# Kernel optimization log

Hardware: AMD Instinct MI355X
Metric: run time of the kernel (lower is better)

The kernel has to match this reference:

```python
import jax, jax.numpy as jnp
import numpy as np
from jax import lax

S = 20      # max_segments
D = 1000    # traj_dict entries
L = 200     # dmp_traj_length
CONV_OUT = 512 * 4 * 4  # 8192 for 100x100 input


def _conv(x, w, b):
    # NCHW valid conv, kernel 3x3, stride 1 (matches nn.Conv2d defaults)
    y = lax.conv_general_dilated(x, w, (1, 1), 'VALID',
                                 dimension_numbers=('NCHW', 'OIHW', 'NCHW'))
    return y + b[None, :, None, None]


def _pool2(x):
    # max_pool2d(kernel=2, stride=2), floor mode == VALID reduce_window
    return lax.reduce_window(x, -jnp.inf, lax.max, (1, 1, 2, 2), (1, 1, 2, 2), 'VALID')


def setup_inputs() -> dict:
    key = jax.random.key(0)
    ks = jax.random.split(key, 20)
    f32 = jnp.float32

    def rn(k, shape, s):
        return jax.random.normal(k, shape, dtype=f32) * s

    x = jax.random.normal(ks[0], (128, 3, 100, 100), dtype=f32)
    w1 = rn(ks[1], (64, 3, 3, 3), 0.1);    b1 = jnp.zeros((64,), f32)
    w2 = rn(ks[2], (128, 64, 3, 3), 0.04); b2 = jnp.zeros((128,), f32)
    w3 = rn(ks[3], (256, 128, 3, 3), 0.03); b3 = jnp.zeros((256,), f32)
    w4 = rn(ks[4], (512, 256, 3, 3), 0.02); b4 = jnp.zeros((512,), f32)
    out_size = 2 + 3 * S
    fw1 = rn(ks[5], (CONV_OUT, 2048), 0.01); fb1 = jnp.zeros((2048,), f32)
    fw2 = rn(ks[6], (2048, 2048), 0.02);     fb2 = jnp.zeros((2048,), f32)
    fw3 = rn(ks[7], (2048, out_size), 0.02); fb3 = jnp.zeros((out_size,), f32)
    traj_dict = jax.random.normal(ks[8], (D, L, 2), dtype=f32)
    return {
        'x': x,
        'w1': w1, 'b1': b1, 'w2': w2, 'b2': b2,
        'w3': w3, 'b3': b3, 'w4': w4, 'b4': b4,
        'fw1': fw1, 'fb1': fb1, 'fw2': fw2, 'fb2': fb2,
        'fw3': fw3, 'fb3': fb3,
        'traj_dict': traj_dict,
    }


def _forward(x, w1, b1, w2, b2, w3, b3, w4, b4,
             fw1, fb1, fw2, fb2, fw3, fb3, traj_dict):
    # conv encoder (relu(maxpool(conv)) x4, matching the torch order)
    h = jax.nn.relu(_pool2(_conv(x, w1, b1)))
    h = jax.nn.relu(_pool2(_conv(h, w2, b2)))
    h = jax.nn.relu(_pool2(_conv(h, w3, b3)))
    h = jax.nn.relu(_pool2(_conv(h, w4, b4)))
    h = h.reshape(h.shape[0], -1)                      # [B, 8192]
    # FC stack: tanh on hidden layers, linear head (dropout p=0 / eval)
    h = jnp.tanh(h @ fw1 + fb1)
    h = jnp.tanh(h @ fw2 + fb2)
    p = h @ fw3 + fb3                                  # [B, 2 + 3S]

    B = p.shape[0]
    init_pos = p[:, :2]                                # [B, 2]
    seg = p[:, 2:].reshape(B, S, 3)                    # (dict_idx, x_scale, y_scale)

    # getTrajFromDict: the loop of round/clamp/sign/abs one-hot masks is exactly
    # a gather at the clamped rounded index (round is half-to-even in both torch and jax)
    idx = jnp.clip(jnp.round(seg[..., 0]), 0, D - 1).astype(jnp.int32)  # [B, S]
    base = traj_dict[idx]                              # [B, S, L, 2]

    scaled = base * seg[:, :, None, 1:3]               # [B, S, L, 2]
    # chain segments: each segment starts at previous segment's endpoint
    offsets = scaled[:, :, -1, :]                      # [B, S, 2]
    starts = init_pos[:, None, :] + jnp.cumsum(offsets, axis=1) - offsets  # exclusive cumsum
    traj = (scaled + starts[:, :, None, :]).reshape(B, S * L, 2)
    return traj


def reference(x, w1, b1, w2, b2, w3, b3, w4, b4,
              fw1, fb1, fw2, fb2, fw3, fb3, traj_dict):
    return _forward(x, w1, b1, w2, b2, w3, b3, w4, b4,
                    fw1, fb1, fw2, fb2, fw3, fb3, traj_dict)
```

## Files before the change

kernel.cpp:

```cpp
#include <hip/hip_runtime.h>
#include <hip/hip_bf16.h>

typedef __attribute__((ext_vector_type(8))) short s8v;
typedef __attribute__((ext_vector_type(4))) float f4v;
typedef unsigned short ushort;
typedef unsigned int uint;

union V8 { s8v v; short s[8]; };

__device__ __forceinline__ short f2bf(float v){
    union { __hip_bfloat16 b; short u; } x;
    x.b = __float2bfloat16(v);
    return x.u;
}
__device__ __forceinline__ float bf2f(short u){
    union { short u; __hip_bfloat16 b; } x;
    x.u = u;
    return __bfloat162float(x.b);
}
__device__ __forceinline__ void splitf(float v, short& h, short& l){
    h = f2bf(v);
    l = f2bf(v - bf2f(h));
}
__device__ __forceinline__ uint packsplit(float v){
    short h, l; splitf(v, h, l);
    return (uint)(ushort)h | ((uint)(ushort)l << 16);
}

template<int CIN, int HIN, int PH, int OCB, int SPT, int OCS, int CICH, int COUT>
__global__ __launch_bounds__(SPT*OCS) void k_conv_pool_relu(
    const float* __restrict__ in, const float* __restrict__ w,
    const float* __restrict__ bias, uint* __restrict__ out)
{
    constexpr int BT    = SPT * OCS;
    constexpr int WIN   = HIN;
    constexpr int PW    = PH;
    constexpr int OCBLK = OCB * OCS;
    constexpr int WSTR  = CICH * 9 + 1;

    __shared__ float wsh[OCBLK * WSTR];

    const int b   = blockIdx.z;
    const int oc0 = blockIdx.y * OCBLK;
    const int t   = threadIdx.x;
    const int spl = (OCS == 1) ? t : (t % SPT);
    const int ocq = (OCS == 1) ? 0 : (t / SPT);
    const int sp  = blockIdx.x * SPT + spl;
    const bool active = sp < PH * PW;
    const int py = active ? (sp / PW) : 0;
    const int px = active ? (sp % PW) : 0;

    float acc[OCB][4];
#pragma unroll
    for (int j = 0; j < OCB; ++j)
        acc[j][0] = acc[j][1] = acc[j][2] = acc[j][3] = 0.f;

    const float* inb = in + (size_t)b * CIN * HIN * WIN;

    for (int c0 = 0; c0 < CIN; c0 += CICH) {
        __syncthreads();
        for (int i = t; i < OCBLK * CICH * 9; i += BT) {
            int j = i / (CICH * 9);
            int r = i - j * (CICH * 9);
            wsh[j * WSTR + r] = w[((size_t)(oc0 + j) * CIN + c0) * 9 + r];
        }
        __syncthreads();

        for (int ci = 0; ci < CICH; ++ci) {
            const float* inc = inb + (size_t)(c0 + ci) * HIN * WIN
                             + (2 * py) * WIN + 2 * px;
            float patch[4][4];
#pragma unroll
            for (int r = 0; r < 4; ++r)
#pragma unroll
                for (int c = 0; c < 4; ++c)
                    patch[r][c] = inc[r * WIN + c];

#pragma unroll
            for (int j = 0; j < OCB; ++j) {
                const float* wp = &wsh[(ocq * OCB + j) * WSTR + ci * 9];
#pragma unroll
                for (int kh = 0; kh < 3; ++kh)
#pragma unroll
                    for (int kw = 0; kw < 3; ++kw) {
                        float wv = wp[kh * 3 + kw];
                        acc[j][0] = fmaf(patch[kh][kw],         wv, acc[j][0]);
                        acc[j][1] = fmaf(patch[kh][kw + 1],     wv, acc[j][1]);
                        acc[j][2] = fmaf(patch[kh + 1][kw],     wv, acc[j][2]);
                        acc[j][3] = fmaf(patch[kh + 1][kw + 1], wv, acc[j][3]);
                    }
            }
        }
    }

    if (active) {
#pragma unroll
        for (int j = 0; j < OCB; ++j) {
            int oc = oc0 + ocq * OCB + j;
            float m = fmaxf(fmaxf(acc[j][0], acc[j][1]),
                            fmaxf(acc[j][2], acc[j][3]));
            m = fmaxf(m + bias[oc], 0.f);
            out[(((size_t)b * COUT + oc) * PH + py) * PW + px] = packsplit(m);
        }
    }
}

__global__ void k_wsplit(const float* __restrict__ w, ushort* __restrict__ oh,
                         ushort* __restrict__ ol, int n)
{
    int i = blockIdx.x * 256 + threadIdx.x;
    if (i < n) {
        short h, l; splitf(w[i], h, l);
        oh[i] = (ushort)h; ol[i] = (ushort)l;
    }
}

__global__ __launch_bounds__(256) void k_wsplitT(
    const float* __restrict__ B, ushort* __restrict__ oh, ushort* __restrict__ ol,
    int K, int N)
{
    __shared__ float tl[32][33];
    const int n0 = blockIdx.x * 32, k0 = blockIdx.y * 32;
    const int r = threadIdx.x >> 5, c = threadIdx.x & 31;
#pragma unroll
    for (int it = 0; it < 4; ++it) {
        int row = r + it * 8;
        tl[row][c] = B[(size_t)(k0 + row) * N + n0 + c];
    }
    __syncthreads();
#pragma unroll
    for (int it = 0; it < 4; ++it) {
        int a = r + it * 8;
        float v = tl[c][a];
        short h, l; splitf(v, h, l);
        size_t o = (size_t)(n0 + a) * K + k0 + c;
        oh[o] = (ushort)h; ol[o] = (ushort)l;
    }
}

template<int MODE, int BPRE, int EPI, int K, int KCH, int N,
         int CIN, int HIN, int PPH, int PPW, int COUT, int TPI>
__global__ __launch_bounds__(256) void k_gemm2(
    const void* __restrict__ A0, const void* __restrict__ A1,
    const void* __restrict__ B0, const void* __restrict__ B1,
    const float* __restrict__ bias, void* __restrict__ O0, void* __restrict__ O1)
{
    __shared__ short Ah[64][40], Al[64][40], Bh[128][40], Bl[128][40];
    __shared__ int offs[MODE == 0 ? K : 1];

    const int t    = threadIdx.x;
    const int lane = t & 63;
    const int wave = t >> 6;
    const int n0   = blockIdx.y * 128;
    const int sArow = t & 63, sAoct = t >> 6;
    const int sBrow = t & 127, sBo = t >> 7;

    const uint*   ArI = nullptr;
    const ushort* Ahg = nullptr;
    const ushort* Alg = nullptr;
    int b = 0, ptile = 0, kbeg = 0, kend = K;

    if (MODE == 0) {
        b = blockIdx.x / TPI;
        ptile = blockIdx.x - b * TPI;
        int pl = ptile * 16 + (sArow >> 2);
        int quad = sArow & 3;
        int py = 0, px = 0;
        if (pl < PPH * PPW) { py = pl / PPW; px = pl - py * PPW; }
        ArI = (const uint*)A0 + (size_t)b * CIN * HIN * HIN
            + (size_t)(2 * py + (quad >> 1)) * HIN + (2 * px + (quad & 1));
        for (int k = t; k < K; k += 256) {
            int ci = k / 9, r = k - ci * 9;
            int kh = r / 3, kw = r - kh * 3;
            offs[k] = ci * HIN * HIN + kh * HIN + kw;
        }
    } else {
        int arow = blockIdx.x * 64 + sArow;
        Ahg = (const ushort*)A0 + (size_t)arow * K;
        Alg = (const ushort*)A1 + (size_t)arow * K;
        kbeg = blockIdx.z * KCH;
        kend = kbeg + KCH;
    }

    f4v acc[2][4];
    const f4v z4 = {0.f, 0.f, 0.f, 0.f};
#pragma unroll
    for (int i = 0; i < 2; ++i)
#pragma unroll
        for (int j = 0; j < 4; ++j) acc[i][j] = z4;

    for (int kk = kbeg; kk < kend; kk += 32) {
        __syncthreads();
        {
            const int kb = kk + sAoct * 8;
            V8 ha, la;
            if (MODE == 0) {
#pragma unroll
                for (int j = 0; j < 8; ++j) {
                    uint v = ArI[offs[kb + j]];
                    ha.s[j] = (short)(v & 0xffffu);
                    la.s[j] = (short)(v >> 16);
                }
            } else {
                ha.v = *(const s8v*)(Ahg + kb);
                la.v = *(const s8v*)(Alg + kb);
            }
            *(s8v*)&Ah[sArow][sAoct * 8] = ha.v;
            *(s8v*)&Al[sArow][sAoct * 8] = la.v;
        }
        {
#pragma unroll
            for (int q = 0; q < 2; ++q) {
                const int o = sBo + 2 * q;
                const int kb = kk + o * 8;
                V8 hb, lb;
                if (BPRE) {
                    hb.v = *(const s8v*)((const ushort*)B0 + (size_t)(n0 + sBrow) * K + kb);
                    lb.v = *(const s8v*)((const ushort*)B1 + (size_t)(n0 + sBrow) * K + kb);
                } else if (MODE == 0) {
                    const float* bp = (const float*)B0 + (size_t)(n0 + sBrow) * K + kb;
                    float4 v0 = *(const float4*)bp;
                    float4 v1 = *(const float4*)(bp + 4);
                    splitf(v0.x, hb.s[0], lb.s[0]); splitf(v0.y, hb.s[1], lb.s[1]);
                    splitf(v0.z, hb.s[2], lb.s[2]); splitf(v0.w, hb.s[3], lb.s[3]);
                    splitf(v1.x, hb.s[4], lb.s[4]); splitf(v1.y, hb.s[5], lb.s[5]);
                    splitf(v1.z, hb.s[6], lb.s[6]); splitf(v1.w, hb.s[7], lb.s[7]);
                } else {
                    const float* bp = (const float*)B0 + (size_t)kb * N + n0 + sBrow;
#pragma unroll
                    for (int j = 0; j < 8; ++j)
                        splitf(bp[(size_t)j * N], hb.s[j], lb.s[j]);
                }
                *(s8v*)&Bh[sBrow][o * 8] = hb.v;
                *(s8v*)&Bl[sBrow][o * 8] = lb.v;
            }
        }
        __syncthreads();

        const int fm = lane & 15;
        const int fk = (lane >> 4) * 8;
        s8v a_h[2], a_l[2], b_h[4], b_l[4];
#pragma unroll
        for (int i = 0; i < 2; ++i) {
            a_h[i] = *(const s8v*)&Ah[(wave & 1) * 32 + i * 16 + fm][fk];
            a_l[i] = *(const s8v*)&Al[(wave & 1) * 32 + i * 16 + fm][fk];
        }
#pragma unroll
        for (int j = 0; j < 4; ++j) {
            b_h[j] = *(const s8v*)&Bh[(wave >> 1) * 64 + j * 16 + fm][fk];
            b_l[j] = *(const s8v*)&Bl[(wave >> 1) * 64 + j * 16 + fm][fk];
        }
#define MF(a_, b_, c_) c_ = __builtin_amdgcn_mfma_f32_16x16x32_bf16(a_, b_, c_, 0, 0, 0)
#pragma unroll
        for (int i = 0; i < 2; ++i)
#pragma unroll
            for (int j = 0; j < 4; ++j) {
                MF(a_h[i], b_h[j], acc[i][j]);
                MF(a_h[i], b_l[j], acc[i][j]);
                MF(a_l[i], b_h[j], acc[i][j]);
            }
#undef MF
    }

    if (MODE == 0) {
        const int PP = PPH * PPW;
#pragma unroll
        for (int i = 0; i < 2; ++i)
#pragma unroll
            for (int j = 0; j < 4; ++j) {
                int p  = ptile * 16 + (wave & 1) * 8 + i * 4 + (lane >> 4);
                int oc = n0 + (wave >> 1) * 64 + j * 16 + (lane & 15);
                if (p < PP) {
                    f4v v = acc[i][j];
                    float m = fmaxf(fmaxf(v.x, v.y), fmaxf(v.z, v.w));
                    m = fmaxf(m + bias[oc], 0.f);
                    size_t o = (size_t)(b * COUT + oc) * PP + p;
                    if (EPI == 0) {
                        ((uint*)O0)[o] = packsplit(m);
                    } else {
                        short h, l; splitf(m, h, l);
                        ((ushort*)O0)[o] = (ushort)h;
                        ((ushort*)O1)[o] = (ushort)l;
                    }
                }
            }
    } else {
        float* P = (float*)O0 + (size_t)blockIdx.z * 128 * N;
#pragma unroll
        for (int i = 0; i < 2; ++i)
#pragma unroll
            for (int j = 0; j < 4; ++j) {
                int n = n0 + (wave >> 1) * 64 + j * 16 + (lane & 15);
                int mb = blockIdx.x * 64 + (wave & 1) * 32 + i * 16 + (lane >> 4) * 4;
                f4v v = acc[i][j];
                P[(size_t)(mb + 0) * N + n] = v.x;
                P[(size_t)(mb + 1) * N + n] = v.y;
                P[(size_t)(mb + 2) * N + n] = v.z;
                P[(size_t)(mb + 3) * N + n] = v.w;
            }
    }
}

template<int EFMT>
__global__ void k_fc_epi2(const float* __restrict__ P, const float* __restrict__ bias,
                          ushort* __restrict__ oh, ushort* __restrict__ ol,
                          float* __restrict__ of, int MN, int N, int KS)
{
    int i = blockIdx.x * 256 + threadIdx.x;
    if (i >= MN) return;
    float s = 0.f;
    for (int z = 0; z < KS; ++z) s += P[(size_t)z * MN + i];
    s = tanhf(s + bias[i % N]);
    if (EFMT == 1) {
        short h, l; splitf(s, h, l);
        oh[i] = (ushort)h; ol[i] = (ushort)l;
    } else {
        of[i] = s;
    }
}

__global__ __launch_bounds__(64) void k_fc3_part(
    const float* __restrict__ A, const float* __restrict__ B,
    float* __restrict__ P, int K, int N, int KS)
{
    const int m = blockIdx.x, kz = blockIdx.y;
    const int n = threadIdx.x;
    const int kchunk = K / KS;
    if (n < N) {
        float acc = 0.f;
        const float* Am = A + (size_t)m * K;
        const int ke = (kz + 1) * kchunk;
        for (int k = kz * kchunk; k < ke; ++k)
            acc = fmaf(Am[k], B[(size_t)k * N + n], acc);
        P[((size_t)kz * 128 + m) * N + n] = acc;
    }
}

__global__ void k_fc_epi(const float* __restrict__ P, const float* __restrict__ bias,
                         float* __restrict__ out, int MN, int N, int KS)
{
    int i = blockIdx.x * 256 + threadIdx.x;
    if (i >= MN) return;
    float s = 0.f;
    for (int z = 0; z < KS; ++z) s += P[(size_t)z * MN + i];
    out[i] = s + bias[i % N];
}

__global__ void k_traj_start(const float* __restrict__ p, const float* __restrict__ td,
                             float* __restrict__ starts, float* __restrict__ sa,
                             int* __restrict__ sidx)
{
    int b = threadIdx.x;
    const float* pb = p + b * 62;
    float cx = pb[0], cy = pb[1];
    for (int s = 0; s < 20; ++s) {
        float f  = pb[2 + 3 * s];
        float a0 = pb[3 + 3 * s];
        float a1 = pb[4 + 3 * s];
        int idx = (int)fminf(fmaxf(rintf(f), 0.f), 999.f);
        int bs = b * 20 + s;
        sidx[bs] = idx;
        sa[bs * 2 + 0] = a0;
        sa[bs * 2 + 1] = a1;
        starts[bs * 2 + 0] = cx;
        starts[bs * 2 + 1] = cy;
        cx += td[((size_t)idx * 200 + 199) * 2 + 0] * a0;
        cy += td[((size_t)idx * 200 + 199) * 2 + 1] * a1;
    }
}

__global__ void k_traj_main(const float* __restrict__ td, const float* __restrict__ starts,
                            const float* __restrict__ sa, const int* __restrict__ sidx,
                            float* __restrict__ out)
{
    int bs = blockIdx.x;
    int idx = sidx[bs];
    float a0 = sa[bs * 2 + 0], a1 = sa[bs * 2 + 1];
    float s0 = starts[bs * 2 + 0], s1 = starts[bs * 2 + 1];
    const float* row = td + (size_t)idx * 400;
    float* o = out + (size_t)bs * 400;
    for (int e = threadIdx.x; e < 400; e += blockDim.x) {
        float v = row[e];
        o[e] = (e & 1) ? fmaf(v, a1, s1) : fmaf(v, a0, s0);
    }
}

template<int BPRE>
static void run_all(void* const* d_in, float* out, char* ws, hipStream_t stream)
{
    const float* x   = (const float*)d_in[0];
    const float* w1  = (const float*)d_in[1];
    const float* b1  = (const float*)d_in[2];
    const float* w2  = (const float*)d_in[3];
    const float* b2  = (const float*)d_in[4];
    const float* w3  = (const float*)d_in[5];
    const float* b3  = (const float*)d_in[6];
    const float* w4  = (const float*)d_in[7];
    const float* b4  = (const float*)d_in[8];
    const float* fw1 = (const float*)d_in[9];
    const float* fb1 = (const float*)d_in[10];
    const float* fw2 = (const float*)d_in[11];
    const float* fb2 = (const float*)d_in[12];
    const float* fw3 = (const float*)d_in[13];
    const float* fb3 = (const float*)d_in[14];
    const float* td  = (const float*)d_in[15];

    uint*   h1   = (uint*)ws;
    uint*   h2   = (uint*)(ws + 78675968ull);
    uint*   h3   = (uint*)ws;
    ushort* fw1h = (ushort*)(ws + 13107200ull);
    ushort* fw1l = (ushort*)(ws + 46661632ull);
    ushort* h4h  = (ushort*)(ws + 80216064ull);
    ushort* h4l  = (ushort*)(ws + 82313216ull);
    ushort* fw2h = (ushort*)(ws + 84410368ull);
    ushort* fw2l = (ushort*)(ws + 92798976ull);
    float*  part = (float*)(ws + 101187584ull);
    ushort* a1h  = (ushort*)(ws + 109576192ull);
    ushort* a1l  = (ushort*)(ws + 110100480ull);
    float*  a2   = (float*)(ws + 110624768ull);
    float*  p    = (float*)(ws + 111673344ull);
    float*  starts = (float*)(ws + 111705088ull);
    float*  sa   = (float*)(ws + 111725568ull);
    int*    sidx = (int*)(ws + 111746048ull);
    ushort* w2h = (ushort*)(ws + 113344512ull);
    ushort* w2l = (ushort*)(ws + 113491968ull);
    ushort* w3h = (ushort*)(ws + 113639424ull);
    ushort* w3l = (ushort*)(ws + 114229248ull);
    ushort* w4h = (ushort*)(ws + 114819072ull);
    ushort* w4l = (ushort*)(ws + 117178368ull);

    if (BPRE) {
        k_wsplit<<<(73728 + 255) / 256, 256, 0, stream>>>(w2, w2h, w2l, 73728);
        k_wsplit<<<(294912 + 255) / 256, 256, 0, stream>>>(w3, w3h, w3l, 294912);
        k_wsplit<<<(1179648 + 255) / 256, 256, 0, stream>>>(w4, w4h, w4l, 1179648);
    }

    k_conv_pool_relu<3, 100, 49, 16, 256, 1, 3, 64>
        <<<dim3(10, 4, 128), 256, 0, stream>>>(x, w1, b1, h1);

    k_gemm2<0, BPRE, 0, 576, 576, 128, 64, 49, 23, 23, 128, 34>
        <<<dim3(34 * 128, 1), 256, 0, stream>>>(
            h1, nullptr, BPRE ? (const void*)w2h : (const void*)w2,
            BPRE ? (const void*)w2l : nullptr, b2, h2, nullptr);
    k_gemm2<0, BPRE, 0, 1152, 1152, 256, 128, 23, 10, 10, 256, 7>
        <<<dim3(7 * 128, 2), 256, 0, stream>>>(
            h2, nullptr, BPRE ? (const void*)w3h : (const void*)w3,
            BPRE ? (const void*)w3l : nullptr, b3, h3, nullptr);

    if (BPRE) {
        k_wsplitT<<<dim3(2048 / 32, 8192 / 32), 256, 0, stream>>>(fw1, fw1h, fw1l, 8192, 2048);
        k_wsplitT<<<dim3(2048 / 32, 2048 / 32), 256, 0, stream>>>(fw2, fw2h, fw2l, 2048, 2048);
    }

    k_gemm2<0, BPRE, 1, 2304, 2304, 512, 256, 10, 4, 4, 512, 1>
        <<<dim3(128, 4), 256, 0, stream>>>(
            h3, nullptr, BPRE ? (const void*)w4h : (const void*)w4,
            BPRE ? (const void*)w4l : nullptr, b4, h4h, h4l);

    k_gemm2<1, BPRE, 2, 8192, 1024, 2048, 0, 1, 1, 1, 1, 1>
        <<<dim3(2, 16, 8), 256, 0, stream>>>(
            h4h, h4l, BPRE ? (const void*)fw1h : (const void*)fw1,
            BPRE ? (const void*)fw1l : nullptr, nullptr, part, nullptr);
    k_fc_epi2<1><<<(128 * 2048 + 255) / 256, 256, 0, stream>>>(
        part, fb1, a1h, a1l, nullptr, 128 * 2048, 2048, 8);
    k_gemm2<1, BPRE, 2, 2048, 256, 2048, 0, 1, 1, 1, 1, 1>
        <<<dim3(2, 16, 8), 256, 0, stream>>>(
            a1h, a1l, BPRE ? (const void*)fw2h : (const void*)fw2,
            BPRE ? (const void*)fw2l : nullptr, nullptr, part, nullptr);
    k_fc_epi2<2><<<(128 * 2048 + 255) / 256, 256, 0, stream>>>(
        part, fb2, nullptr, nullptr, a2, 128 * 2048, 2048, 8);

    k_fc3_part<<<dim3(128, 4), 64, 0, stream>>>(a2, fw3, part, 2048, 62, 4);
    k_fc_epi<<<(128 * 62 + 255) / 256, 256, 0, stream>>>(
        part, fb3, p, 128 * 62, 62, 4);
    k_traj_start<<<1, 128, 0, stream>>>(p, td, starts, sa, sidx);
    k_traj_main<<<2560, 256, 0, stream>>>(td, starts, sa, sidx, out);
}

extern "C" void kernel_launch(void* const* d_in, const int* in_sizes, int n_in,
                              void* d_out, int out_size, void* d_ws, size_t ws_size,
                              hipStream_t stream)
{
    (void)in_sizes; (void)n_in; (void)out_size;
    if (ws_size >= 119537664ull)
        run_all<1>(d_in, (float*)d_out, (char*)d_ws, stream);
    else
        run_all<0>(d_in, (float*)d_out, (char*)d_ws, stream);
}
```

Baseline: 1.084 ms.

## Reorder conv im2col K to tap-major and prefetch next K tile into registers

Changes the im2col K ordering for the conv GEMMs from channel-major to tap-major (k = r*CIN + ci), so each 8-wide K chunk covers 8 consecutive channels at one tap. The shared offset table and its integer-division setup go away, and the weight split kernel permutes weights to match. It also adds register double-buffering: global loads for the next 32-wide K tile are issued before the MFMA work on the current tile, hiding load latency at the cost of extra registers. With the non-pre-split weight path, B loads become strided by 9 instead of float4 vectors.

```diff
diff --git a/kernel.cpp b/kernel.cpp
--- a/kernel.cpp
+++ b/kernel.cpp
@@ -105,13 +105,19 @@
     }
 }
 
-__global__ void k_wsplit(const float* __restrict__ w, ushort* __restrict__ oh,
-                         ushort* __restrict__ ol, int n)
+__global__ void k_wsplit_perm(const float* __restrict__ w, ushort* __restrict__ oh,
+                              ushort* __restrict__ ol, int CIN, int total)
 {
     int i = blockIdx.x * 256 + threadIdx.x;
-    if (i < n) {
+    if (i < total) {
+        int K = CIN * 9;
+        int n = i / K;
+        int rem = i - n * K;
+        int ci = rem / 9;
+        int r = rem - 9 * ci;
         short h, l; splitf(w[i], h, l);
-        oh[i] = (ushort)h; ol[i] = (ushort)l;
+        size_t o = (size_t)n * K + r * CIN + ci;
+        oh[o] = (ushort)h; ol[o] = (ushort)l;
     }
 }
 
@@ -138,15 +144,17 @@
     }
 }
 
-template<int MODE, int BPRE, int EPI, int K, int KCH, int N,
-         int CIN, int HIN, int PPH, int PPW, int COUT, int TPI>
-__global__ __launch_bounds__(256) void k_gemm2(
+template<int MODE, int BPRE, int EPI, int LOG2CIN, int K, int KCH, int N,
+         int HIN, int PPH, int PPW, int COUT, int TPI>
+__global__ __launch_bounds__(256) void k_gemm3(
     const void* __restrict__ A0, const void* __restrict__ A1,
     const void* __restrict__ B0, const void* __restrict__ B1,
     const float* __restrict__ bias, void* __restrict__ O0, void* __restrict__ O1)
 {
+    constexpr int CIN = 1 << LOG2CIN;
+    constexpr int HH  = HIN * HIN;
+
     __shared__ short Ah[64][40], Al[64][40], Bh[128][40], Bl[128][40];
-    __shared__ int offs[MODE == 0 ? K : 1];
 
     const int t    = threadIdx.x;
     const int lane = t & 63;
@@ -167,13 +175,8 @@
         int quad = sArow & 3;
         int py = 0, px = 0;
         if (pl < PPH * PPW) { py = pl / PPW; px = pl - py * PPW; }
-        ArI = (const uint*)A0 + (size_t)b * CIN * HIN * HIN
+        ArI = (const uint*)A0 + (size_t)b * CIN * HH
             + (size_t)(2 * py + (quad >> 1)) * HIN + (2 * px + (quad & 1));
-        for (int k = t; k < K; k += 256) {
-            int ci = k / 9, r = k - ci * 9;
-            int kh = r / 3, kw = r - kh * 3;
-            offs[k] = ci * HIN * HIN + kh * HIN + kw;
-        }
     } else {
         int arow = blockIdx.x * 64 + sArow;
         Ahg = (const ushort*)A0 + (size_t)arow * K;
@@ -182,6 +185,50 @@
         kend = kbeg + KCH;
     }
 
+    auto pfA = [&](int kkx, V8& ha, V8& la) {
+        const int kb = kkx + sAoct * 8;
+        if (MODE == 0) {
+            const int r  = kb >> LOG2CIN;
+            const int cb = kb & (CIN - 1);
+            const int rh = (r * 11) >> 5;
+            const int rw = r - 3 * rh;
+            const uint* g = ArI + (size_t)cb * HH + rh * HIN + rw;
+#pragma unroll
+            for (int j = 0; j < 8; ++j) {
+                uint v = g[(size_t)j * HH];
+                ha.s[j] = (short)(v & 0xffffu);
+                la.s[j] = (short)(v >> 16);
+            }
+        } else {
+            ha.v = *(const s8v*)(Ahg + kb);
+            la.v = *(const s8v*)(Alg + kb);
+        }
+    };
+    auto pfB = [&](int kkx, V8* hb, V8* lb) {
+#pragma unroll
+        for (int q = 0; q < 2; ++q) {
+            const int o = sBo + 2 * q;
+            const int kb = kkx + o * 8;
+            if (BPRE) {
+                hb[q].v = *(const s8v*)((const ushort*)B0 + (size_t)(n0 + sBrow) * K + kb);
+                lb[q].v = *(const s8v*)((const ushort*)B1 + (size_t)(n0 + sBrow) * K + kb);
+            } else if (MODE == 0) {
+                const int r  = kb >> LOG2CIN;
+                const int cb = kb & (CIN - 1);
+                const float* bp = (const float*)B0
+                    + (size_t)(n0 + sBrow) * K + (size_t)cb * 9 + r;
+#pragma unroll
+                for (int j = 0; j < 8; ++j)
+                    splitf(bp[9 * j], hb[q].s[j], lb[q].s[j]);
+            } else {
+                const float* bp = (const float*)B0 + (size_t)kb * N + n0 + sBrow;
+#pragma unroll
+                for (int j = 0; j < 8; ++j)
+                    splitf(bp[(size_t)j * N], hb[q].s[j], lb[q].s[j]);
+            }
+        }
+    };
+
     f4v acc[2][4];
     const f4v z4 = {0.f, 0.f, 0.f, 0.f};
 #pragma unroll
@@ -189,51 +236,23 @@
 #pragma unroll
         for (int j = 0; j < 4; ++j) acc[i][j] = z4;
 
+    V8 pAh, pAl, pBh[2], pBl[2];
+    pfA(kbeg, pAh, pAl);
+    pfB(kbeg, pBh, pBl);
+
     for (int kk = kbeg; kk < kend; kk += 32) {
         __syncthreads();
-        {
-            const int kb = kk + sAoct * 8;
-            V8 ha, la;
-            if (MODE == 0) {
-#pragma unroll
-                for (int j = 0; j < 8; ++j) {
-                    uint v = ArI[offs[kb + j]];
-                    ha.s[j] = (short)(v & 0xffffu);
-                    la.s[j] = (short)(v >> 16);
-                }
-            } else {
-                ha.v = *(const s8v*)(Ahg + kb);
-                la.v = *(const s8v*)(Alg + kb);
-            }
-            *(s8v*)&Ah[sArow][sAoct * 8] = ha.v;
-            *(s8v*)&Al[sArow][sAoct * 8] = la.v;
-        }
-        {
-#pragma unroll
-            for (int q = 0; q < 2; ++q) {
-                const int o = sBo + 2 * q;
-                const int kb = kk + o * 8;
-                V8 hb, lb;
-                if (BPRE) {
-                    hb.v = *(const s8v*)((const ushort*)B0 + (size_t)(n0 + sBrow) * K + kb);
-                    lb.v = *(const s8v*)((const ushort*)B1 + (size_t)(n0 + sBrow) * K + kb);
-                } else if (MODE == 0) {
-                    const float* bp = (const float*)B0 + (size_t)(n0 + sBrow) * K + kb;
-                    float4 v0 = *(const float4*)bp;
-                    float4 v1 = *(const float4*)(bp + 4);
-                    splitf(v0.x, hb.s[0], lb.s[0]); splitf(v0.y, hb.s[1], lb.s[1]);
-                    splitf(v0.z, hb.s[2], lb.s[2]); splitf(v0.w, hb.s[3], lb.s[3]);
-                    splitf(v1.x, hb.s[4], lb.s[4]); splitf(v1.y, hb.s[5], lb.s[5]);
-                    splitf(v1.z, hb.s[6], lb.s[6]); splitf(v1.w, hb.s[7], lb.s[7]);
-                } else {
-                    const float* bp = (const float*)B0 + (size_t)kb * N + n0 + sBrow;
-#pragma unroll
-                    for (int j = 0; j < 8; ++j)
-                        splitf(bp[(size_t)j * N], hb.s[j], lb.s[j]);
-                }
-                *(s8v*)&Bh[sBrow][o * 8] = hb.v;
-                *(s8v*)&Bl[sBrow][o * 8] = lb.v;
-            }
+        *(s8v*)&Ah[sArow][sAoct * 8] = pAh.v;
+        *(s8v*)&Al[sArow][sAoct * 8] = pAl.v;
+#pragma unroll
+        for (int q = 0; q < 2; ++q) {
+            const int o = sBo + 2 * q;
+            *(s8v*)&Bh[sBrow][o * 8] = pBh[q].v;
+            *(s8v*)&Bl[sBrow][o * 8] = pBl[q].v;
+        }
+        if (kk + 32 < kend) {
+            pfA(kk + 32, pAh, pAl);
+            pfB(kk + 32, pBh, pBl);
         }
         __syncthreads();
 
@@ -430,19 +449,19 @@
     ushort* w4l = (ushort*)(ws + 117178368ull);
 
     if (BPRE) {
-        k_wsplit<<<(73728 + 255) / 256, 256, 0, stream>>>(w2, w2h, w2l, 73728);
-        k_wsplit<<<(294912 + 255) / 256, 256, 0, stream>>>(w3, w3h, w3l, 294912);
-        k_wsplit<<<(1179648 + 255) / 256, 256, 0, stream>>>(w4, w4h, w4l, 1179648);
+        k_wsplit_perm<<<(73728 + 255) / 256, 256, 0, stream>>>(w2, w2h, w2l, 64, 73728);
+        k_wsplit_perm<<<(294912 + 255) / 256, 256, 0, stream>>>(w3, w3h, w3l, 128, 294912);
+        k_wsplit_perm<<<(1179648 + 255) / 256, 256, 0, stream>>>(w4, w4h, w4l, 256, 1179648);
     }
 
     k_conv_pool_relu<3, 100, 49, 16, 256, 1, 3, 64>
         <<<dim3(10, 4, 128), 256, 0, stream>>>(x, w1, b1, h1);
 
-    k_gemm2<0, BPRE, 0, 576, 576, 128, 64, 49, 23, 23, 128, 34>
+    k_gemm3<0, BPRE, 0, 6, 576, 576, 128, 49, 23, 23, 128, 34>
         <<<dim3(34 * 128, 1), 256, 0, stream>>>(
             h1, nullptr, BPRE ? (const void*)w2h : (const void*)w2,
             BPRE ? (const void*)w2l : nullptr, b2, h2, nullptr);
-    k_gemm2<0, BPRE, 0, 1152, 1152, 256, 128, 23, 10, 10, 256, 7>
+    k_gemm3<0, BPRE, 0, 7, 1152, 1152, 256, 23, 10, 10, 256, 7>
         <<<dim3(7 * 128, 2), 256, 0, stream>>>(
             h2, nullptr, BPRE ? (const void*)w3h : (const void*)w3,
             BPRE ? (const void*)w3l : nullptr, b3, h3, nullptr);
@@ -452,18 +471,18 @@
         k_wsplitT<<<dim3(2048 / 32, 2048 / 32), 256, 0, stream>>>(fw2, fw2h, fw2l, 2048, 2048);
     }
 
-    k_gemm2<0, BPRE, 1, 2304, 2304, 512, 256, 10, 4, 4, 512, 1>
+    k_gemm3<0, BPRE, 1, 8, 2304, 2304, 512, 10, 4, 4, 512, 1>
         <<<dim3(128, 4), 256, 0, stream>>>(
             h3, nullptr, BPRE ? (const void*)w4h : (const void*)w4,
             BPRE ? (const void*)w4l : nullptr, b4, h4h, h4l);
 
-    k_gemm2<1, BPRE, 2, 8192, 1024, 2048, 0, 1, 1, 1, 1, 1>
+    k_gemm3<1, BPRE, 2, 0, 8192, 1024, 2048, 1, 1, 1, 1, 1>
         <<<dim3(2, 16, 8), 256, 0, stream>>>(
             h4h, h4l, BPRE ? (const void*)fw1h : (const void*)fw1,
             BPRE ? (const void*)fw1l : nullptr, nullptr, part, nullptr);
     k_fc_epi2<1><<<(128 * 2048 + 255) / 256, 256, 0, stream>>>(
         part, fb1, a1h, a1l, nullptr, 128 * 2048, 2048, 8);
-    k_gemm2<1, BPRE, 2, 2048, 256, 2048, 0, 1, 1, 1, 1, 1>
+    k_gemm3<1, BPRE, 2, 0, 2048, 256, 2048, 1, 1, 1, 1, 1>
         <<<dim3(2, 16, 8), 256, 0, stream>>>(
             a1h, a1l, BPRE ? (const void*)fw2h : (const void*)fw2,
             BPRE ? (const void*)fw2l : nullptr, nullptr, part, nullptr);
```

Result: no change. 1.077 ms (-0.6%).
